# Optimization experiments

Measured on AMD Instinct MI355X. Metric: run time of the kernel, lower is better.

Reference implementation:

```python
import jax, jax.numpy as jnp
import numpy as np

LAMBDA_C = 10.0
LAMBDA_E = 10.0
LAMBDA_O = 10.0
H = 0.1          # proximity / thickness scale from __init__ h=0.1
EPS = 1e-8


def _pairwise_sq(a, b):
    # a [N,3], b [M,3] -> [N,M] squared distances
    return jnp.sum((a[:, None, :] - b[None, :, :]) ** 2, axis=-1)


def _total_loss(pred_vertices, face_probs, target_vertices, pred_faces, target_faces):
    pv, tv, probs = pred_vertices, target_vertices, face_probs

    # ---- chamfer loss (bidirectional mean of NN squared distances) ----
    d2_pt = _pairwise_sq(pv, tv)                       # [N, M]
    chamfer = d2_pt.min(axis=1).mean() + d2_pt.min(axis=0).mean()

    # ---- probabilistic surface distance via face barycenters ----
    tri = pv[pred_faces]                               # [F,3,3]
    ttri = tv[target_faces]                            # [Ft,3,3]
    bp = tri.mean(axis=1)                              # [F,3]
    bt = ttri.mean(axis=1)                             # [Ft,3]
    d2_f = _pairwise_sq(bp, bt)                        # [F,Ft]
    surface = (probs * d2_f.min(axis=1)).mean() + d2_f.min(axis=0).mean()

    # ---- shared pairwise geometry ----
    v0, v1, v2 = tri[:, 0], tri[:, 1], tri[:, 2]
    n = jnp.cross(v1 - v0, v2 - v0)                    # [F,3] face normals
    nhat = n / (jnp.linalg.norm(n, axis=-1, keepdims=True) + EPS)
    F_ = tri.shape[0]
    mask = 1.0 - jnp.eye(F_, dtype=pv.dtype)           # exclude self pairs
    cd2 = _pairwise_sq(bp, bp)                         # [F,F] centroid dist^2
    gate = jnp.exp(-cd2 / H)                           # soft spatial proximity gate

    # ---- triangle collision: vertices of tri j vs plane of tri i ----
    # s[i,j,v] = nhat_i . (tri[j,v] - v0_i)
    s = jnp.einsum('id,fvd->ifv', nhat, tri) - jnp.einsum('id,id->i', nhat, v0)[:, None, None]
    pen_col = jax.nn.relu(-(s.max(-1) * s.min(-1)))    # >0 iff tri j straddles plane i
    collision = (probs[:, None] * mask * gate * pen_col).sum() / F_

    # ---- edge crossing: segment-segment closest distance, all 9 edge pairs ----
    p = tri                                            # edge starts [F,3,3]
    q = jnp.roll(tri, -1, axis=1)                      # edge ends   [F,3,3]
    p1 = p[:, None, :, None, :]                        # [F,1,3,1,3]
    q1 = q[:, None, :, None, :]
    p2 = p[None, :, None, :, :]                        # [1,F,1,3,3]
    q2 = q[None, :, None, :, :]
    d1 = q1 - p1
    d2 = q2 - p2
    r = p1 - p2
    a = jnp.sum(d1 * d1, -1)
    e = jnp.sum(d2 * d2, -1)
    f = jnp.sum(d2 * r, -1)
    c = jnp.sum(d1 * r, -1)
    b = jnp.sum(d1 * d2, -1)
    denom = a * e - b * b
    sseg = jnp.clip((b * f - c * e) / (denom + EPS), 0.0, 1.0)
    tseg = jnp.clip((b * sseg + f) / (e + EPS), 0.0, 1.0)
    sseg = jnp.clip((b * tseg - c) / (a + EPS), 0.0, 1.0)
    cp1 = p1 + sseg[..., None] * d1
    cp2 = p2 + tseg[..., None] * d2
    dist = jnp.sqrt(jnp.sum((cp1 - cp2) ** 2, -1) + EPS)   # [F,F,3,3]
    pen_edge = jax.nn.relu(H - dist).sum((-1, -2))          # [F,F]
    edge_crossing = (probs[:, None] * mask * gate * pen_edge).sum() / F_

    # ---- triangle overlap: centroid of tri j close to plane of tri i ----
    dp = jnp.abs(jnp.einsum('id,jd->ij', nhat, bp) - jnp.einsum('id,id->i', nhat, v0)[:, None])
    pen_ov = jax.nn.relu(H - dp)                            # [F,F]
    overlap = (probs[:, None] * mask * gate * pen_ov).sum() / F_

    return (chamfer + surface
            + LAMBDA_C * collision
            + LAMBDA_E * edge_crossing
            + LAMBDA_O * overlap)


def setup_inputs() -> dict:
    key = jax.random.key(0)
    k1, k2, k3, k4, k5 = jax.random.split(key, 5)
    N, F, M, Ft = 512, 1024, 32768, 65536
    return {
        'pred_vertices': jax.random.normal(k1, (N, 3), dtype=jnp.float32),
        'face_probs': jax.random.uniform(k2, (F,), dtype=jnp.float32),
        'target_vertices': jax.random.normal(k3, (M, 3), dtype=jnp.float32),
        'pred_faces': jax.random.randint(k4, (F, 3), 0, N),
        'target_faces': jax.random.randint(k5, (Ft, 3), 0, M),
    }


def reference(pred_vertices, face_probs, target_vertices, pred_faces, target_faces):
    return _total_loss(pred_vertices, face_probs, target_vertices, pred_faces, target_faces)
```

## Files before the change

### kernel.cpp

```cpp
#include <hip/hip_runtime.h>
#include <hip/hip_bf16.h>
#include <math.h>

#define EPSF 1e-8f
#define HPARAM 0.1f
#define TI 4
#define FCH 128

__device__ __forceinline__ float waveReduceSum(float v) {
#pragma unroll
    for (int o = 32; o > 0; o >>= 1) v += __shfl_down(v, o, 64);
    return v;
}
__device__ __forceinline__ float blockSum(float s, float* red4) {
    s = waveReduceSum(s);
    int lane = threadIdx.x & 63, wid = threadIdx.x >> 6;
    if (lane == 0) red4[wid] = s;
    __syncthreads();
    return red4[0] + red4[1] + red4[2] + red4[3];
}
__device__ __forceinline__ float clamp01(float x) {
    return fminf(fmaxf(x, 0.0f), 1.0f);
}

__global__ __launch_bounds__(256) void k_pre(
    const float* __restrict__ pv, const int* __restrict__ pf,
    const float* __restrict__ tv, const int* __restrict__ tf,
    float* __restrict__ tri, float4* __restrict__ bp4,
    float* __restrict__ nhat, float* __restrict__ d0,
    float4* __restrict__ bt4, float4* __restrict__ tv4, float4* __restrict__ pv4,
    int N, int F, int M, int Ft)
{
    int nbF = (F + 255) >> 8, nbFt = (Ft + 255) >> 8, nbM = (M + 255) >> 8;
    int b = blockIdx.x, tid = threadIdx.x;
    if (b < nbF) {
        int i = b * 256 + tid;
        if (i >= F) return;
        int a = pf[i * 3 + 0], bb = pf[i * 3 + 1], c = pf[i * 3 + 2];
        float v0x = pv[a * 3], v0y = pv[a * 3 + 1], v0z = pv[a * 3 + 2];
        float v1x = pv[bb * 3], v1y = pv[bb * 3 + 1], v1z = pv[bb * 3 + 2];
        float v2x = pv[c * 3], v2y = pv[c * 3 + 1], v2z = pv[c * 3 + 2];
        tri[i * 9 + 0] = v0x; tri[i * 9 + 1] = v0y; tri[i * 9 + 2] = v0z;
        tri[i * 9 + 3] = v1x; tri[i * 9 + 4] = v1y; tri[i * 9 + 5] = v1z;
        tri[i * 9 + 6] = v2x; tri[i * 9 + 7] = v2y; tri[i * 9 + 8] = v2z;
        float bx = (v0x + v1x + v2x) / 3.0f;
        float by = (v0y + v1y + v2y) / 3.0f;
        float bz = (v0z + v1z + v2z) / 3.0f;
        bp4[i] = make_float4(bx, by, bz, bx * bx + by * by + bz * bz);
        float e1x = v1x - v0x, e1y = v1y - v0y, e1z = v1z - v0z;
        float e2x = v2x - v0x, e2y = v2y - v0y, e2z = v2z - v0z;
        float nx = e1y * e2z - e1z * e2y;
        float ny = e1z * e2x - e1x * e2z;
        float nz = e1x * e2y - e1y * e2x;
        float nrm = sqrtf(nx * nx + ny * ny + nz * nz);
        float inv = 1.0f / (nrm + EPSF);
        float hx = nx * inv, hy = ny * inv, hz = nz * inv;
        nhat[i * 3 + 0] = hx; nhat[i * 3 + 1] = hy; nhat[i * 3 + 2] = hz;
        d0[i] = hx * v0x + hy * v0y + hz * v0z;
    } else if (b < nbF + nbFt) {
        int j = (b - nbF) * 256 + tid;
        if (j >= Ft) return;
        int a = tf[j * 3 + 0], bb = tf[j * 3 + 1], c = tf[j * 3 + 2];
        float bx = (tv[a * 3 + 0] + tv[bb * 3 + 0] + tv[c * 3 + 0]) / 3.0f;
        float by = (tv[a * 3 + 1] + tv[bb * 3 + 1] + tv[c * 3 + 1]) / 3.0f;
        float bz = (tv[a * 3 + 2] + tv[bb * 3 + 2] + tv[c * 3 + 2]) / 3.0f;
        bt4[j] = make_float4(bx, by, bz, bx * bx + by * by + bz * bz);
    } else if (b < nbF + nbFt + nbM) {
        int j = (b - nbF - nbFt) * 256 + tid;
        if (j >= M) return;
        float x = tv[j * 3], y = tv[j * 3 + 1], z = tv[j * 3 + 2];
        tv4[j] = make_float4(x, y, z, x * x + y * y + z * z);
    } else {
        int j = (b - nbF - nbFt - nbM) * 256 + tid;
        if (j >= N) return;
        float x = pv[j * 3], y = pv[j * 3 + 1], z = pv[j * 3 + 2];
        pv4[j] = make_float4(x, y, z, x * x + y * y + z * z);
    }
}

__global__ __launch_bounds__(256) void k_mega(
    const float4* __restrict__ pv4, const float4* __restrict__ tv4,
    const float* __restrict__ tri, const float4* __restrict__ bp4,
    const float* __restrict__ nhat, const float* __restrict__ d0,
    const float* __restrict__ probs, const float4* __restrict__ bt4,
    float* __restrict__ chamFp, float* __restrict__ chamBp,
    float* __restrict__ surfFp, float* __restrict__ surfBp,
    float* __restrict__ pairp,
    int N, int F, int M, int Ft, int o1, int o2)
{
    __shared__ float4 sh4[576];
    __shared__ int slist[256];
    __shared__ int scnt[4];
    __shared__ float red4[4];
    int b = blockIdx.x;
    int tid = threadIdx.x;

    if (b < o1) {
        int NTG = Ft >> 11;
        int fc = b / NTG, tg = b % NTG;
        float4* sF = sh4;
        unsigned* sMin = (unsigned*)(sh4 + FCH);
        if (tid < FCH) {
            float4 p = bp4[fc * FCH + tid];
            sF[tid] = p;
            sMin[tid] = __float_as_uint(3.4e38f);
        }
        __syncthreads();
        int j0 = tg * 2048 + tid;
        float4 t8[8]; float mm[8];
#pragma unroll
        for (int u = 0; u < 8; ++u) { t8[u] = bt4[j0 + u * 256]; mm[u] = 3.4e38f; }
        for (int k = 0; k < FCH; ++k) {
            int fi = (k + tid) & (FCH - 1);
            float4 p = sF[fi];
            float px2 = -2.0f * p.x, py2 = -2.0f * p.y, pz2 = -2.0f * p.z;
            float m8 = 3.4e38f;
#pragma unroll
            for (int u = 0; u < 8; ++u) {
                float acc = fmaf(px2, t8[u].x, fmaf(py2, t8[u].y, fmaf(pz2, t8[u].z, p.w + t8[u].w)));
                mm[u] = fminf(mm[u], acc);
                m8 = fminf(m8, acc);
            }
            atomicMin(&sMin[fi], __float_as_uint(fmaxf(m8, 0.0f)));
        }
#pragma unroll
        for (int u = 0; u < 8; ++u) surfBp[fc * Ft + j0 + u * 256] = mm[u];
        __syncthreads();
        if (tid < FCH) surfFp[tg * F + fc * FCH + tid] = __uint_as_float(sMin[tid]);
    } else if (b < o2) {
        int rb = b - o1;
        int MTG = M >> 11;
        int vc = rb / MTG, tg = rb % MTG;
        float4* sF = sh4;
        unsigned* sMin = (unsigned*)(sh4 + FCH);
        if (tid < FCH) {
            float4 p = pv4[vc * FCH + tid];
            sF[tid] = p;
            sMin[tid] = __float_as_uint(3.4e38f);
        }
        __syncthreads();
        int j0 = tg * 2048 + tid;
        float4 t8[8]; float mm[8];
#pragma unroll
        for (int u = 0; u < 8; ++u) { t8[u] = tv4[j0 + u * 256]; mm[u] = 3.4e38f; }
        for (int k = 0; k < FCH; ++k) {
            int fi = (k + tid) & (FCH - 1);
            float4 p = sF[fi];
            float px2 = -2.0f * p.x, py2 = -2.0f * p.y, pz2 = -2.0f * p.z;
            float m8 = 3.4e38f;
#pragma unroll
            for (int u = 0; u < 8; ++u) {
                float acc = fmaf(px2, t8[u].x, fmaf(py2, t8[u].y, fmaf(pz2, t8[u].z, p.w + t8[u].w)));
                mm[u] = fminf(mm[u], acc);
                m8 = fminf(m8, acc);
            }
            atomicMin(&sMin[fi], __float_as_uint(fmaxf(m8, 0.0f)));
        }
#pragma unroll
        for (int u = 0; u < 8; ++u) chamBp[vc * M + j0 + u * 256] = mm[u];
        __syncthreads();
        if (tid < FCH) chamFp[tg * N + vc * FCH + tid] = __uint_as_float(sMin[tid]);
    } else {
        int rb = b - o2;
        int bpF = F >> 8;
        int ig = rb / bpF;
        int fg = rb % bpF;
        float* sTri = (float*)sh4;
        for (int t = tid; t < 256 * 9; t += 256) sTri[t] = tri[fg * 256 * 9 + t];
        __syncthreads();

        int lane = tid & 63, wid = tid >> 6;
        float contrib = 0.0f;
#pragma unroll 1
        for (int ii = 0; ii < TI; ++ii) {
            int i = ig * TI + ii;
            float ti[9];
#pragma unroll
            for (int v = 0; v < 9; ++v) ti[v] = tri[i * 9 + v];
            float nix = nhat[i * 3], niy = nhat[i * 3 + 1], niz = nhat[i * 3 + 2];
            float di = d0[i];
            float4 bi = bp4[i];
            float pi = probs[i];
            float p1xa[3], p1ya[3], p1za[3], d1xa[3], d1ya[3], d1za[3], ava[3], rava[3];
#pragma unroll
            for (int e1 = 0; e1 < 3; ++e1) {
                int e1n = (e1 == 2) ? 0 : e1 + 1;
                p1xa[e1] = ti[e1 * 3]; p1ya[e1] = ti[e1 * 3 + 1]; p1za[e1] = ti[e1 * 3 + 2];
                d1xa[e1] = ti[e1n * 3] - p1xa[e1];
                d1ya[e1] = ti[e1n * 3 + 1] - p1ya[e1];
                d1za[e1] = ti[e1n * 3 + 2] - p1za[e1];
                ava[e1] = d1xa[e1] * d1xa[e1] + d1ya[e1] * d1ya[e1] + d1za[e1] * d1za[e1];
                rava[e1] = __builtin_amdgcn_rcpf(ava[e1] + EPSF);
            }
            int f = fg * 256 + tid;
            float4 bft = bp4[f];
            float cdx = bi.x - bft.x, cdy = bi.y - bft.y, cdz = bi.z - bft.z;
            float cd2 = cdx * cdx + cdy * cdy + cdz * cdz;
            bool pass = (f != i) && (cd2 <= 2.0f);
            unsigned long long mask = __ballot(pass);
            if (lane == 0) scnt[wid] = __popcll(mask);
            __syncthreads();
            int base = 0;
#pragma unroll
            for (int w = 0; w < 4; ++w) base += (w < wid) ? scnt[w] : 0;
            int nCand = scnt[0] + scnt[1] + scnt[2] + scnt[3];
            int pfx = __popcll(mask & ((1ULL << lane) - 1ULL));
            if (pass) slist[base + pfx] = tid;
            __syncthreads();

            if (tid < nCand) {
                int src = slist[tid];
                float4 bf = bp4[fg * 256 + src];
                float rcx = bi.x - bf.x, rcy = bi.y - bf.y, rcz = bi.z - bf.z;
                float gate = __expf(-10.0f * (rcx * rcx + rcy * rcy + rcz * rcz));
                float tf9[9];
#pragma unroll
                for (int v = 0; v < 9; ++v) tf9[v] = sTri[src * 9 + v];
                float s0 = nix * tf9[0] + niy * tf9[1] + niz * tf9[2] - di;
                float s1 = nix * tf9[3] + niy * tf9[4] + niz * tf9[5] - di;
                float s2 = nix * tf9[6] + niy * tf9[7] + niz * tf9[8] - di;
                float smax = fmaxf(fmaxf(s0, s1), s2);
                float smin = fminf(fminf(s0, s1), s2);
                float pen_col = fmaxf(-(smax * smin), 0.0f);
                float dp = fabsf(nix * bf.x + niy * bf.y + niz * bf.z - di);
                float pen_ov = fmaxf(HPARAM - dp, 0.0f);
                float q2x[3], q2y[3], q2z[3], e2xa[3], e2ya[3], e2za[3], eva[3], reva[3];
#pragma unroll
                for (int e2 = 0; e2 < 3; ++e2) {
                    int e2n = (e2 == 2) ? 0 : e2 + 1;
                    q2x[e2] = tf9[e2 * 3]; q2y[e2] = tf9[e2 * 3 + 1]; q2z[e2] = tf9[e2 * 3 + 2];
                    e2xa[e2] = tf9[e2n * 3] - q2x[e2];
                    e2ya[e2] = tf9[e2n * 3 + 1] - q2y[e2];
                    e2za[e2] = tf9[e2n * 3 + 2] - q2z[e2];
                    eva[e2] = e2xa[e2] * e2xa[e2] + e2ya[e2] * e2ya[e2] + e2za[e2] * e2za[e2];
                    reva[e2] = __builtin_amdgcn_rcpf(eva[e2] + EPSF);
                }
                float d2v[9];
                float dminv = 3.4e38f;
#pragma unroll
                for (int e1 = 0; e1 < 3; ++e1) {
#pragma unroll
                    for (int e2 = 0; e2 < 3; ++e2) {
                        float rx = p1xa[e1] - q2x[e2], ry = p1ya[e1] - q2y[e2], rz = p1za[e1] - q2z[e2];
                        float f_ = e2xa[e2] * rx + e2ya[e2] * ry + e2za[e2] * rz;
                        float c_ = d1xa[e1] * rx + d1ya[e1] * ry + d1za[e1] * rz;
                        float b_ = d1xa[e1] * e2xa[e2] + d1ya[e1] * e2ya[e2] + d1za[e1] * e2za[e2];
                        float denom = ava[e1] * eva[e2] - b_ * b_;
                        float rden = __builtin_amdgcn_rcpf(denom + EPSF);
                        float ss = clamp01(fmaf(-c_, eva[e2], b_ * f_) * rden);
                        float tt = clamp01(fmaf(b_, ss, f_) * reva[e2]);
                        ss = clamp01(fmaf(b_, tt, -c_) * rava[e1]);
                        float vx = fmaf(ss, d1xa[e1], p1xa[e1]) - fmaf(tt, e2xa[e2], q2x[e2]);
                        float vy = fmaf(ss, d1ya[e1], p1ya[e1]) - fmaf(tt, e2ya[e2], q2y[e2]);
                        float vz = fmaf(ss, d1za[e1], p1za[e1]) - fmaf(tt, e2za[e2], q2z[e2]);
                        float dd = vx * vx + vy * vy + vz * vz;
                        d2v[e1 * 3 + e2] = dd;
                        dminv = fminf(dminv, dd);
                    }
                }
                float pen_edge = 0.0f;
                if (dminv + EPSF < HPARAM * HPARAM) {
#pragma unroll
                    for (int qq = 0; qq < 9; ++qq)
                        pen_edge += fmaxf(HPARAM - __builtin_amdgcn_sqrtf(d2v[qq] + EPSF), 0.0f);
                }
                contrib += pi * gate * (pen_col + pen_ov + pen_edge);
            }
            __syncthreads();
        }
        float s = blockSum(contrib, red4);
        if (tid == 0) pairp[rb] = s;
    }
}

__global__ __launch_bounds__(256) void k_reduce(
    const float* __restrict__ surfBp, int Ft, int ncS, float invFt,
    const float* __restrict__ chamBp, int M, int ncC, float invM,
    const float* __restrict__ chamFp, int N, int nGV, float invN,
    const float* __restrict__ surfFp, const float* __restrict__ probs, int F, int nGF, float invF,
    const float* __restrict__ pairp, int nPB, float pairScale,
    float* __restrict__ smallp)
{
    __shared__ float red4[4];
    int b = blockIdx.x, tid = threadIdx.x;
    int nbS = Ft >> 8, nbC = M >> 8, nbA = N >> 8, nbSA = F >> 8;
    float s;
    if (b < nbS) {
        int j = b * 256 + tid;
        float r = 3.4e38f;
        for (int c = 0; c < ncS; ++c) r = fminf(r, surfBp[c * Ft + j]);
        s = r * invFt;
    } else if (b < nbS + nbC) {
        int j = (b - nbS) * 256 + tid;
        float r = 3.4e38f;
        for (int c = 0; c < ncC; ++c) r = fminf(r, chamBp[c * M + j]);
        s = r * invM;
    } else if (b < nbS + nbC + nbA) {
        int v = (b - nbS - nbC) * 256 + tid;
        float r = 3.4e38f;
        for (int c = 0; c < nGV; ++c) r = fminf(r, chamFp[c * N + v]);
        s = r * invN;
    } else if (b < nbS + nbC + nbA + nbSA) {
        int i = (b - nbS - nbC - nbA) * 256 + tid;
        float r = 3.4e38f;
        for (int c = 0; c < nGF; ++c) r = fminf(r, surfFp[c * F + i]);
        s = probs[i] * r * invF;
    } else {
        int t = (b - nbS - nbC - nbA - nbSA) * 256 + tid;
        s = (t < nPB) ? pairp[t] * pairScale : 0.0f;
    }
    float r = blockSum(s, red4);
    if (tid == 0) smallp[b] = r;
}

__global__ __launch_bounds__(256) void k_fin(
    const float* __restrict__ smallp, int n, float* __restrict__ out)
{
    __shared__ float red4[4];
    float s = 0.0f;
    for (int t = threadIdx.x; t < n; t += 256) s += smallp[t];
    float r = blockSum(s, red4);
    if (threadIdx.x == 0) out[0] = r;
}

extern "C" void kernel_launch(void* const* d_in, const int* in_sizes, int n_in,
                              void* d_out, int out_size, void* d_ws, size_t ws_size,
                              hipStream_t stream) {
    const float* pv    = (const float*)d_in[0];
    const float* probs = (const float*)d_in[1];
    const float* tv    = (const float*)d_in[2];
    const int*   pf    = (const int*)d_in[3];
    const int*   tf    = (const int*)d_in[4];
    float* out = (float*)d_out;

    int N  = in_sizes[0] / 3;
    int F  = in_sizes[1];
    int M  = in_sizes[2] / 3;
    int Ft = in_sizes[4] / 3;

    int bpF = F >> 8;
    int nPB = (F / TI) * bpF;

    int NFC = F / FCH;
    int NVC = N / FCH;
    int NTG = Ft >> 11;
    int MTG = M >> 11;

    float* ws = (float*)d_ws;
    float* w_tri    = ws;
    float* w_nhat   = w_tri + F * 9;
    float* w_d0     = w_nhat + F * 3;
    float4* w_bp4   = (float4*)(w_d0 + F);
    float4* w_bt4   = w_bp4 + F;
    float4* w_tv4   = w_bt4 + Ft;
    float4* w_pv4   = w_tv4 + M;
    float* w_chamFp = (float*)(w_pv4 + N);
    float* w_surfFp = w_chamFp + MTG * N;
    float* w_pair   = w_surfFp + NTG * F;
    float* w_small  = w_pair + nPB;
    float* w_surfBp = w_small + 512;
    float* w_chamBp = w_surfBp + (size_t)NFC * Ft;

    int o1 = NFC * NTG;
    int o2 = o1 + NVC * MTG;
    int gTot = o2 + nPB;

    int nSmall = (Ft >> 8) + (M >> 8) + (N >> 8) + (F >> 8) + ((nPB + 255) >> 8);
    int gPre = (F + 255) / 256 + (Ft + 255) / 256 + (M + 255) / 256 + (N + 255) / 256;

    k_pre<<<gPre, 256, 0, stream>>>(
        pv, pf, tv, tf, w_tri, w_bp4, w_nhat, w_d0, w_bt4, w_tv4, w_pv4,
        N, F, M, Ft);
    k_mega<<<gTot, 256, 0, stream>>>(
        w_pv4, w_tv4, w_tri, w_bp4, w_nhat, w_d0, probs, w_bt4,
        w_chamFp, w_chamBp, w_surfFp, w_surfBp, w_pair,
        N, F, M, Ft, o1, o2);
    k_reduce<<<nSmall, 256, 0, stream>>>(
        w_surfBp, Ft, NFC, 1.0f / (float)Ft,
        w_chamBp, M, NVC, 1.0f / (float)M,
        w_chamFp, N, MTG, 1.0f / (float)N,
        w_surfFp, probs, F, NTG, 1.0f / (float)F,
        w_pair, nPB, 10.0f / (float)F,
        w_small);
    k_fin<<<1, 256, 0, stream>>>(w_small, nSmall, out);
}
```

Before: 54.50 us.

## Replace LDS atomicMin with wave-shuffle min and halve predicate chunk size

The two nearest-neighbour branches (surface and chamfer) are merged into one generic code path. The per-iteration shared-memory atomicMin with rotated indexing becomes a wave-level xor-shuffle min, with one store per wave that a final pass combines. The -2 scaling is folded into the shared predicate array. The predicate chunk shrinks from 128 to 64, which doubles the number of blocks and the size of the partial-minimum buffers written and later re-read by the reduce kernel.

```diff
diff --git a/kernel.cpp b/kernel.cpp
--- a/kernel.cpp
+++ b/kernel.cpp
@@ -5,7 +5,8 @@
 #define EPSF 1e-8f
 #define HPARAM 0.1f
 #define TI 4
-#define FCH 128
+#define PCH 64
+#define TT 8
 
 __device__ __forceinline__ float waveReduceSum(float v) {
 #pragma unroll
@@ -94,72 +95,59 @@
     __shared__ float red4[4];
     int b = blockIdx.x;
     int tid = threadIdx.x;
-
-    if (b < o1) {
-        int NTG = Ft >> 11;
-        int fc = b / NTG, tg = b % NTG;
+    int lane = tid & 63, wid = tid >> 6;
+
+    if (b < o2) {
+        const float4* __restrict__ P;
+        const float4* __restrict__ T;
+        float* __restrict__ Fp;
+        float* __restrict__ Bp;
+        int fc, tg, npred, ntgt;
+        if (b < o1) {
+            int NTG = Ft >> 11;
+            fc = b / NTG; tg = b % NTG;
+            P = bp4; T = bt4; Fp = surfFp; Bp = surfBp;
+            npred = F; ntgt = Ft;
+        } else {
+            int rb = b - o1;
+            int MTG = M >> 11;
+            fc = rb / MTG; tg = rb % MTG;
+            P = pv4; T = tv4; Fp = chamFp; Bp = chamBp;
+            npred = N; ntgt = M;
+        }
         float4* sF = sh4;
-        unsigned* sMin = (unsigned*)(sh4 + FCH);
-        if (tid < FCH) {
-            float4 p = bp4[fc * FCH + tid];
-            sF[tid] = p;
-            sMin[tid] = __float_as_uint(3.4e38f);
+        float* wMin = (float*)slist;
+        if (tid < PCH) {
+            float4 p = P[fc * PCH + tid];
+            sF[tid] = make_float4(-2.0f * p.x, -2.0f * p.y, -2.0f * p.z, p.w);
         }
         __syncthreads();
         int j0 = tg * 2048 + tid;
-        float4 t8[8]; float mm[8];
-#pragma unroll
-        for (int u = 0; u < 8; ++u) { t8[u] = bt4[j0 + u * 256]; mm[u] = 3.4e38f; }
-        for (int k = 0; k < FCH; ++k) {
-            int fi = (k + tid) & (FCH - 1);
-            float4 p = sF[fi];
-            float px2 = -2.0f * p.x, py2 = -2.0f * p.y, pz2 = -2.0f * p.z;
+        float4 t8[TT]; float mm[TT];
+#pragma unroll
+        for (int u = 0; u < TT; ++u) { t8[u] = T[j0 + u * 256]; mm[u] = 3.4e38f; }
+        for (int k = 0; k < PCH; ++k) {
+            float4 p = sF[k];
             float m8 = 3.4e38f;
 #pragma unroll
-            for (int u = 0; u < 8; ++u) {
-                float acc = fmaf(px2, t8[u].x, fmaf(py2, t8[u].y, fmaf(pz2, t8[u].z, p.w + t8[u].w)));
-                mm[u] = fminf(mm[u], acc);
-                m8 = fminf(m8, acc);
+            for (int u = 0; u < TT; ++u) {
+                float a = fmaf(p.x, t8[u].x, fmaf(p.y, t8[u].y, fmaf(p.z, t8[u].z, p.w)));
+                float d2 = a + t8[u].w;
+                mm[u] = fminf(mm[u], d2);
+                m8 = fminf(m8, d2);
             }
-            atomicMin(&sMin[fi], __float_as_uint(fmaxf(m8, 0.0f)));
-        }
-#pragma unroll
-        for (int u = 0; u < 8; ++u) surfBp[fc * Ft + j0 + u * 256] = mm[u];
+#pragma unroll
+            for (int o = 32; o > 0; o >>= 1) m8 = fminf(m8, __shfl_xor(m8, o, 64));
+            if (lane == 0) wMin[k * 4 + wid] = m8;
+        }
+#pragma unroll
+        for (int u = 0; u < TT; ++u) Bp[fc * ntgt + j0 + u * 256] = mm[u];
         __syncthreads();
-        if (tid < FCH) surfFp[tg * F + fc * FCH + tid] = __uint_as_float(sMin[tid]);
-    } else if (b < o2) {
-        int rb = b - o1;
-        int MTG = M >> 11;
-        int vc = rb / MTG, tg = rb % MTG;
-        float4* sF = sh4;
-        unsigned* sMin = (unsigned*)(sh4 + FCH);
-        if (tid < FCH) {
-            float4 p = pv4[vc * FCH + tid];
-            sF[tid] = p;
-            sMin[tid] = __float_as_uint(3.4e38f);
-        }
-        __syncthreads();
-        int j0 = tg * 2048 + tid;
-        float4 t8[8]; float mm[8];
-#pragma unroll
-        for (int u = 0; u < 8; ++u) { t8[u] = tv4[j0 + u * 256]; mm[u] = 3.4e38f; }
-        for (int k = 0; k < FCH; ++k) {
-            int fi = (k + tid) & (FCH - 1);
-            float4 p = sF[fi];
-            float px2 = -2.0f * p.x, py2 = -2.0f * p.y, pz2 = -2.0f * p.z;
-            float m8 = 3.4e38f;
-#pragma unroll
-            for (int u = 0; u < 8; ++u) {
-                float acc = fmaf(px2, t8[u].x, fmaf(py2, t8[u].y, fmaf(pz2, t8[u].z, p.w + t8[u].w)));
-                mm[u] = fminf(mm[u], acc);
-                m8 = fminf(m8, acc);
-            }
-            atomicMin(&sMin[fi], __float_as_uint(fmaxf(m8, 0.0f)));
-        }
-#pragma unroll
-        for (int u = 0; u < 8; ++u) chamBp[vc * M + j0 + u * 256] = mm[u];
-        __syncthreads();
-        if (tid < FCH) chamFp[tg * N + vc * FCH + tid] = __uint_as_float(sMin[tid]);
+        if (tid < PCH) {
+            float r = fminf(fminf(wMin[tid * 4], wMin[tid * 4 + 1]),
+                            fminf(wMin[tid * 4 + 2], wMin[tid * 4 + 3]));
+            Fp[tg * npred + fc * PCH + tid] = r;
+        }
     } else {
         int rb = b - o2;
         int bpF = F >> 8;
@@ -169,7 +157,6 @@
         for (int t = tid; t < 256 * 9; t += 256) sTri[t] = tri[fg * 256 * 9 + t];
         __syncthreads();
 
-        int lane = tid & 63, wid = tid >> 6;
         float contrib = 0.0f;
 #pragma unroll 1
         for (int ii = 0; ii < TI; ++ii) {
@@ -274,10 +261,10 @@
 }
 
 __global__ __launch_bounds__(256) void k_reduce(
-    const float* __restrict__ surfBp, int Ft, int ncS, float invFt,
-    const float* __restrict__ chamBp, int M, int ncC, float invM,
-    const float* __restrict__ chamFp, int N, int nGV, float invN,
-    const float* __restrict__ surfFp, const float* __restrict__ probs, int F, int nGF, float invF,
+    const float* __restrict__ surfBp, int Ft, int nFC, float invFt,
+    const float* __restrict__ chamBp, int M, int nVC, float invM,
+    const float* __restrict__ chamFp, int N, int nMTG, float invN,
+    const float* __restrict__ surfFp, const float* __restrict__ probs, int F, int nNTG, float invF,
     const float* __restrict__ pairp, int nPB, float pairScale,
     float* __restrict__ smallp)
 {
@@ -288,22 +275,22 @@
     if (b < nbS) {
         int j = b * 256 + tid;
         float r = 3.4e38f;
-        for (int c = 0; c < ncS; ++c) r = fminf(r, surfBp[c * Ft + j]);
+        for (int c = 0; c < nFC; ++c) r = fminf(r, surfBp[c * Ft + j]);
         s = r * invFt;
     } else if (b < nbS + nbC) {
         int j = (b - nbS) * 256 + tid;
         float r = 3.4e38f;
-        for (int c = 0; c < ncC; ++c) r = fminf(r, chamBp[c * M + j]);
+        for (int c = 0; c < nVC; ++c) r = fminf(r, chamBp[c * M + j]);
         s = r * invM;
     } else if (b < nbS + nbC + nbA) {
         int v = (b - nbS - nbC) * 256 + tid;
         float r = 3.4e38f;
-        for (int c = 0; c < nGV; ++c) r = fminf(r, chamFp[c * N + v]);
+        for (int c = 0; c < nMTG; ++c) r = fminf(r, chamFp[c * N + v]);
         s = r * invN;
     } else if (b < nbS + nbC + nbA + nbSA) {
         int i = (b - nbS - nbC - nbA) * 256 + tid;
         float r = 3.4e38f;
-        for (int c = 0; c < nGF; ++c) r = fminf(r, surfFp[c * F + i]);
+        for (int c = 0; c < nNTG; ++c) r = fminf(r, surfFp[c * F + i]);
         s = probs[i] * r * invF;
     } else {
         int t = (b - nbS - nbC - nbA - nbSA) * 256 + tid;
@@ -341,8 +328,8 @@
     int bpF = F >> 8;
     int nPB = (F / TI) * bpF;
 
-    int NFC = F / FCH;
-    int NVC = N / FCH;
+    int NFC = F / PCH;
+    int NVC = N / PCH;
     int NTG = Ft >> 11;
     int MTG = M >> 11;
 
```

New measurement: 55.26 us. Within noise of the previous version (+1.4%).
